# Kernel optimization log

Hardware: AMD Instinct MI355X
Metric: run time of the kernel (lower is better)

The kernel has to match this reference:

```python
import jax, jax.numpy as jnp
import numpy as np

N_NODES = 100000
N_EDGES = 400000
IN_F, HID, OUT_F = 128, 1024, 64


def gcn_conv(x, src, dst, ew, W, b, n):
    # PyG GCNConv: add self-loops (weight 1), symmetric normalization,
    # out[dst] += norm * (x @ W)[src], then bias.
    loop = jnp.arange(n)
    s = jnp.concatenate([src, loop])
    d = jnp.concatenate([dst, loop])
    w = jnp.concatenate([ew, jnp.ones((n,), dtype=ew.dtype)])
    deg = jax.ops.segment_sum(w, d, num_segments=n)
    dinv = jnp.where(deg > 0, jax.lax.rsqrt(deg), 0.0)
    norm = dinv[s] * w * dinv[d]                      # [E+N]
    h = x @ W                                         # [N, out]
    out = jax.ops.segment_sum(h[s] * norm[:, None], d, num_segments=n)
    return out + b


def setup_inputs() -> dict:
    key = jax.random.key(0)
    k = jax.random.split(key, 8)
    x = jax.random.normal(k[0], (N_NODES, IN_F), dtype=jnp.float32)
    edge_index = jax.random.randint(k[1], (2, N_EDGES), 0, N_NODES, dtype=jnp.int64)
    edge_weight = jax.random.uniform(k[2], (N_EDGES,), dtype=jnp.float32)
    # Glorot-ish init for params
    W1 = jax.random.normal(k[3], (IN_F, HID), dtype=jnp.float32) * (1.0 / np.sqrt(IN_F))
    b1 = jnp.zeros((HID,), dtype=jnp.float32)
    W2 = jax.random.normal(k[4], (HID, OUT_F), dtype=jnp.float32) * (1.0 / np.sqrt(HID))
    b2 = jnp.zeros((OUT_F,), dtype=jnp.float32)
    return {"x": x, "edge_index": edge_index, "edge_weight": edge_weight,
            "W1": W1, "b1": b1, "W2": W2, "b2": b2}


def reference(x, edge_index, edge_weight, W1, b1, W2, b2):
    src, dst = edge_index[0], edge_index[1]
    h = gcn_conv(x, src, dst, edge_weight, W1, b1, N_NODES)
    h = jax.nn.relu(h)
    # F.dropout with training=False is identity (eval mode)
    out = gcn_conv(h, src, dst, edge_weight, W2, b2, N_NODES)
    return out
```

## Files before the change

### kernel.cpp

```cpp
#include <hip/hip_runtime.h>
#include <hip/hip_bf16.h>

#define N_NODES 100000
#define N_EDGES 400000
#define IN_F    128
#define HID     1024
#define OUT_F   64
#define BUCKET_CAP 24

typedef __attribute__((ext_vector_type(8))) short short8;
typedef __attribute__((ext_vector_type(4))) float floatx4;

__device__ inline unsigned short f2bf(float f) {
    unsigned int u = __float_as_uint(f);
    unsigned int r = u + 0x7FFF + ((u >> 16) & 1);
    return (unsigned short)(r >> 16);
}

__device__ inline float bf2f(unsigned int lo16) {
    return __uint_as_float(lo16 << 16);
}

__device__ __forceinline__ void gload_lds16(const void* g, void* l) {
    __builtin_amdgcn_global_load_lds(
        (const __attribute__((address_space(1))) void*)g,
        (__attribute__((address_space(3))) void*)l, 16, 0, 0);
}


__global__ void init_kernel(float* __restrict__ deg, int* __restrict__ cnt, int n) {
    int i = blockIdx.x * blockDim.x + threadIdx.x;
    if (i < n) { deg[i] = 1.0f; cnt[i] = 0; }
}

__global__ void deg_accum_kernel(const int* __restrict__ dst, const float* __restrict__ w,
                                 float* __restrict__ deg, int E) {
    int e = blockIdx.x * blockDim.x + threadIdx.x;
    if (e < E) atomicAdd(&deg[dst[e]], w[e]);
}

__global__ void rsqrt_inplace_kernel(float* __restrict__ deg, int n) {
    int i = blockIdx.x * blockDim.x + threadIdx.x;
    if (i < n) deg[i] = rsqrtf(deg[i]);
}

__global__ void fill_pairs_kernel(const int* __restrict__ src, const int* __restrict__ dst,
                                  const float* __restrict__ w, const float* __restrict__ dinv,
                                  int* __restrict__ cnt, int2* __restrict__ pairs, int E) {
    int e = blockIdx.x * blockDim.x + threadIdx.x;
    if (e < E) {
        int s = src[e];
        int d = dst[e];
        float nv = dinv[s] * w[e] * dinv[d];
        int slot = atomicAdd(&cnt[d], 1);
        if (slot < BUCKET_CAP)
            pairs[(long)d * BUCKET_CAP + slot] = make_int2(s, __float_as_int(nv));
    }
}


__global__ __launch_bounds__(256) void gather128_kernel(
    const int2* __restrict__ pairs, const int* __restrict__ cnt,
    const float* __restrict__ dinv, const float* __restrict__ feat,
    unsigned short* __restrict__ xab)
{
    int node = blockIdx.x * 4 + (threadIdx.x >> 6);
    int l = threadIdx.x & 63;
    float di = dinv[node];
    float s = di * di;
    float2 acc = ((const float2*)(feat + (long)node * IN_F))[l];
    acc.x *= s; acc.y *= s;
    int c = cnt[node]; c = c < BUCKET_CAP ? c : BUCKET_CAP;
    const int2* p = pairs + (long)node * BUCKET_CAP;
    int j = 0;
    for (; j + 4 <= c; j += 4) {
        int2 p0 = p[j], p1 = p[j + 1], p2 = p[j + 2], p3 = p[j + 3];
        float2 v0 = ((const float2*)(feat + (long)p0.x * IN_F))[l];
        float2 v1 = ((const float2*)(feat + (long)p1.x * IN_F))[l];
        float2 v2 = ((const float2*)(feat + (long)p2.x * IN_F))[l];
        float2 v3 = ((const float2*)(feat + (long)p3.x * IN_F))[l];
        float n0 = __int_as_float(p0.y), n1 = __int_as_float(p1.y);
        float n2 = __int_as_float(p2.y), n3 = __int_as_float(p3.y);
        acc.x += n0 * v0.x + n1 * v1.x + n2 * v2.x + n3 * v3.x;
        acc.y += n0 * v0.y + n1 * v1.y + n2 * v2.y + n3 * v3.y;
    }
    for (; j < c; j++) {
        int2 pp = p[j];
        float nv = __int_as_float(pp.y);
        float2 v = ((const float2*)(feat + (long)pp.x * IN_F))[l];
        acc.x += nv * v.x; acc.y += nv * v.y;
    }
    unsigned int pk = (unsigned int)f2bf(acc.x) | ((unsigned int)f2bf(acc.y) << 16);
    ((unsigned int*)(xab + (long)node * IN_F))[l] = pk;
}

__global__ __launch_bounds__(256) void gather64_kernel(
    const int2* __restrict__ pairs, const int* __restrict__ cnt,
    const float* __restrict__ dinv, const unsigned short* __restrict__ tb,
    const float* __restrict__ bias, float* __restrict__ out)
{
    int node = blockIdx.x * 8 + (threadIdx.x >> 5);
    int l = threadIdx.x & 31;
    float di = dinv[node];
    float s = di * di;
    unsigned int tv = ((const unsigned int*)(tb + (long)node * OUT_F))[l];
    float2 bb = ((const float2*)bias)[l];
    float2 acc;
    acc.x = bf2f(tv & 0xffffu) * s + bb.x;
    acc.y = bf2f(tv >> 16) * s + bb.y;
    int c = cnt[node]; c = c < BUCKET_CAP ? c : BUCKET_CAP;
    const int2* p = pairs + (long)node * BUCKET_CAP;
    int j = 0;
    for (; j + 4 <= c; j += 4) {
        int2 p0 = p[j], p1 = p[j + 1], p2 = p[j + 2], p3 = p[j + 3];
        unsigned int u0 = ((const unsigned int*)(tb + (long)p0.x * OUT_F))[l];
        unsigned int u1 = ((const unsigned int*)(tb + (long)p1.x * OUT_F))[l];
        unsigned int u2 = ((const unsigned int*)(tb + (long)p2.x * OUT_F))[l];
        unsigned int u3 = ((const unsigned int*)(tb + (long)p3.x * OUT_F))[l];
        float n0 = __int_as_float(p0.y), n1 = __int_as_float(p1.y);
        float n2 = __int_as_float(p2.y), n3 = __int_as_float(p3.y);
        acc.x += n0 * bf2f(u0 & 0xffffu) + n1 * bf2f(u1 & 0xffffu)
               + n2 * bf2f(u2 & 0xffffu) + n3 * bf2f(u3 & 0xffffu);
        acc.y += n0 * bf2f(u0 >> 16) + n1 * bf2f(u1 >> 16)
               + n2 * bf2f(u2 >> 16) + n3 * bf2f(u3 >> 16);
    }
    for (; j < c; j++) {
        int2 pp = p[j];
        float nv = __int_as_float(pp.y);
        unsigned int u = ((const unsigned int*)(tb + (long)pp.x * OUT_F))[l];
        acc.x += nv * bf2f(u & 0xffffu);
        acc.y += nv * bf2f(u >> 16);
    }
    ((float2*)(out + (long)node * OUT_F))[l] = acc;
}


__global__ void convert_wstream_kernel(const float* __restrict__ W1, const float* __restrict__ W2,
                                       unsigned short* __restrict__ S) {
    int r = blockIdx.x * blockDim.x + threadIdx.x;
    int c = blockIdx.y;
    int f = r >> 9;
    int l = (r >> 3) & 63;
    int j = r & 7;
    float v;
    if (f < 16) {
        int nt = f >> 2, kt = f & 3;
        int hid = c * 64 + nt * 16 + (l & 15);
        int k   = kt * 32 + (l >> 4) * 8 + j;
        v = W1[(long)k * HID + hid];
    } else {
        int f2 = f - 16;
        int kb = f2 >> 2, nt = f2 & 3;
        int kh = c * 64 + kb * 32 + (l >> 4) * 8 + j;
        int oc = nt * 16 + (l & 15);
        v = W2[(long)kh * OUT_F + oc];
    }
    S[(long)c * 12288 + r] = f2bf(v);
}


__global__ __launch_bounds__(512, 2) void fused_mlp_mfma_kernel(
    const unsigned short* __restrict__ Xb, const unsigned short* __restrict__ Wstream,
    const float* __restrict__ b1, unsigned short* __restrict__ Tb, int M)
{
    __shared__ unsigned short Wbuf[2][12288];
    __shared__ unsigned short Hs[8][2048];

    const int tid = threadIdx.x;
    const int w   = tid >> 6;
    const int l   = tid & 63;
    const int lr  = l & 15;
    const int lq  = l >> 4;
    const int swz = (lr & 7) << 4;
    const long row0 = (long)blockIdx.x * 256 + w * 32;

    short8 bx[2][4];
    #pragma unroll
    for (int rt = 0; rt < 2; rt++) {
        long row = row0 + rt * 16 + lr;
        if (row < M) {
            const unsigned short* p = Xb + row * IN_F + lq * 8;
            #pragma unroll
            for (int kt = 0; kt < 4; kt++)
                bx[rt][kt] = *(const short8*)(p + kt * 32);
        } else {
            #pragma unroll
            for (int kt = 0; kt < 4; kt++)
                #pragma unroll
                for (int j = 0; j < 8; j++) bx[rt][kt][j] = 0;
        }
    }

    {
        const unsigned short* g = Wstream + (long)(w * 3) * 512 + l * 8;
        unsigned short* d = &Wbuf[0][(w * 3) * 512];
        #pragma unroll
        for (int s = 0; s < 3; s++)
            gload_lds16(g + s * 512, d + s * 512);
    }
    __syncthreads();

    floatx4 tacc[2][4];
    #pragma unroll
    for (int rt = 0; rt < 2; rt++)
        #pragma unroll
        for (int nt = 0; nt < 4; nt++)
            tacc[rt][nt] = (floatx4)0.0f;

    for (int c = 0; c < 16; c++) {
        const int cur = c & 1;

        if (c < 15) {
            const unsigned short* g = Wstream + (long)(c + 1) * 12288 + (long)(w * 3) * 512 + l * 8;
            unsigned short* d = &Wbuf[cur ^ 1][(w * 3) * 512];
            #pragma unroll
            for (int s = 0; s < 3; s++)
                gload_lds16(g + s * 512, d + s * 512);
        }

        const unsigned short* Wb = &Wbuf[cur][0];

        floatx4 hacc[2][4];
        #pragma unroll
        for (int rt = 0; rt < 2; rt++)
            #pragma unroll
            for (int nt = 0; nt < 4; nt++)
                hacc[rt][nt] = (floatx4)0.0f;

        #pragma unroll
        for (int nt = 0; nt < 4; nt++) {
            short8 w1f[4];
            #pragma unroll
            for (int kt = 0; kt < 4; kt++)
                w1f[kt] = *(const short8*)(Wb + (nt * 4 + kt) * 512 + l * 8);
            #pragma unroll
            for (int kt = 0; kt < 4; kt++) {
                hacc[0][nt] = __builtin_amdgcn_mfma_f32_16x16x32_bf16(w1f[kt], bx[0][kt], hacc[0][nt], 0, 0, 0);
                hacc[1][nt] = __builtin_amdgcn_mfma_f32_16x16x32_bf16(w1f[kt], bx[1][kt], hacc[1][nt], 0, 0, 0);
            }
        }

        char* slab = (char*)&Hs[w][0];
        #pragma unroll
        for (int nt = 0; nt < 4; nt++) {
            floatx4 bb = *(const floatx4*)(b1 + c * 64 + nt * 16 + lq * 4);
            #pragma unroll
            for (int rt = 0; rt < 2; rt++) {
                float h0 = fmaxf(hacc[rt][nt][0] + bb[0], 0.0f);
                float h1 = fmaxf(hacc[rt][nt][1] + bb[1], 0.0f);
                float h2 = fmaxf(hacc[rt][nt][2] + bb[2], 0.0f);
                float h3 = fmaxf(hacc[rt][nt][3] + bb[3], 0.0f);
                unsigned int p0 = (unsigned int)f2bf(h0) | ((unsigned int)f2bf(h1) << 16);
                unsigned int p1 = (unsigned int)f2bf(h2) | ((unsigned int)f2bf(h3) << 16);
                int off = (rt * 16 + lr) * 128 + (((nt * 32) + lq * 8) ^ swz);
                *(uint2*)(slab + off) = make_uint2(p0, p1);
            }
        }

        short8 hf[2][2];
        #pragma unroll
        for (int rt = 0; rt < 2; rt++)
            #pragma unroll
            for (int kb = 0; kb < 2; kb++) {
                int off = (rt * 16 + lr) * 128 + ((kb * 64 + lq * 16) ^ swz);
                hf[rt][kb] = *(const short8*)(slab + off);
            }

        #pragma unroll
        for (int kb = 0; kb < 2; kb++) {
            #pragma unroll
            for (int nt = 0; nt < 4; nt++) {
                short8 w2f = *(const short8*)(Wb + (16 + kb * 4 + nt) * 512 + l * 8);
                tacc[0][nt] = __builtin_amdgcn_mfma_f32_16x16x32_bf16(w2f, hf[0][kb], tacc[0][nt], 0, 0, 0);
                tacc[1][nt] = __builtin_amdgcn_mfma_f32_16x16x32_bf16(w2f, hf[1][kb], tacc[1][nt], 0, 0, 0);
            }
        }

        if (c < 15) __syncthreads();
    }

    #pragma unroll
    for (int rt = 0; rt < 2; rt++) {
        long row = row0 + rt * 16 + lr;
        if (row < M) {
            #pragma unroll
            for (int nt = 0; nt < 4; nt++) {
                unsigned int q0 = (unsigned int)f2bf(tacc[rt][nt][0]) | ((unsigned int)f2bf(tacc[rt][nt][1]) << 16);
                unsigned int q1 = (unsigned int)f2bf(tacc[rt][nt][2]) | ((unsigned int)f2bf(tacc[rt][nt][3]) << 16);
                *(uint2*)(Tb + row * OUT_F + nt * 16 + lq * 4) = make_uint2(q0, q1);
            }
        }
    }
}


extern "C" void kernel_launch(void* const* d_in, const int* in_sizes, int n_in,
                              void* d_out, int out_size, void* d_ws, size_t ws_size,
                              hipStream_t stream) {
    const float* x   = (const float*)d_in[0];
    const int*   src = (const int*)d_in[1];
    const int*   dst = ((const int*)d_in[1]) + N_EDGES;
    const float* ew  = (const float*)d_in[2];
    const float* W1  = (const float*)d_in[3];
    const float* b1  = (const float*)d_in[4];
    const float* W2  = (const float*)d_in[5];
    const float* b2  = (const float*)d_in[6];
    float* out = (float*)d_out;

    float* ws     = (float*)d_ws;
    float* dinv   = ws;
    int*   cnt    = (int*)(ws + 100096);
    int2*  pairs  = (int2*)(ws + 200192);
    unsigned short* xab = (unsigned short*)(ws + 5000192);
    unsigned short* tb  = (unsigned short*)(ws + 11400192);
    unsigned short* wstream = (unsigned short*)(ws + 14600192);

    const int B = 256;

    init_kernel<<<(N_NODES + B - 1) / B, B, 0, stream>>>(dinv, cnt, N_NODES);
    deg_accum_kernel<<<(N_EDGES + B - 1) / B, B, 0, stream>>>(dst, ew, dinv, N_EDGES);
    convert_wstream_kernel<<<dim3(48, 16), B, 0, stream>>>(W1, W2, wstream);
    rsqrt_inplace_kernel<<<(N_NODES + B - 1) / B, B, 0, stream>>>(dinv, N_NODES);
    fill_pairs_kernel<<<(N_EDGES + B - 1) / B, B, 0, stream>>>(src, dst, ew, dinv, cnt, pairs, N_EDGES);

    gather128_kernel<<<N_NODES / 4, 256, 0, stream>>>(pairs, cnt, dinv, x, xab);

    fused_mlp_mfma_kernel<<<(N_NODES + 255) / 256, 512, 0, stream>>>(
        xab, wstream, b1, tb, N_NODES);

    gather64_kernel<<<N_NODES / 8, 256, 0, stream>>>(pairs, cnt, dinv, tb, b2, out);
}
```

Baseline: 182.0 us.

## Pre-convert x to bf16 for gather and double rows per wave in fused MLP

Adds a kernel that converts the input features to bf16 once, so the first-layer neighbour gather reads half as many bytes per edge. The fused MLP kernel now processes 64 rows per wave (512 per block) instead of 32. Each W1/W2 fragment loaded from LDS is reused across four row tiles, and the hidden accumulator is restructured per output-column tile to keep register use bounded. The cost is an extra conversion pass over x and more LDS and register pressure, which may lower occupancy. Grid size halves, to about 196 blocks for 100k nodes.

```diff
diff --git a/kernel.cpp b/kernel.cpp
--- a/kernel.cpp
+++ b/kernel.cpp
@@ -59,36 +59,55 @@
 }
 
 
+__global__ void convert_xb_kernel(const float* __restrict__ in, unsigned short* __restrict__ out, long n8) {
+    long i = (long)blockIdx.x * blockDim.x + threadIdx.x;
+    if (i < n8) {
+        float4 a = ((const float4*)in)[i * 2];
+        float4 b = ((const float4*)in)[i * 2 + 1];
+        unsigned int q0 = (unsigned int)f2bf(a.x) | ((unsigned int)f2bf(a.y) << 16);
+        unsigned int q1 = (unsigned int)f2bf(a.z) | ((unsigned int)f2bf(a.w) << 16);
+        unsigned int q2 = (unsigned int)f2bf(b.x) | ((unsigned int)f2bf(b.y) << 16);
+        unsigned int q3 = (unsigned int)f2bf(b.z) | ((unsigned int)f2bf(b.w) << 16);
+        ((uint4*)out)[i] = make_uint4(q0, q1, q2, q3);
+    }
+}
+
+
 __global__ __launch_bounds__(256) void gather128_kernel(
     const int2* __restrict__ pairs, const int* __restrict__ cnt,
-    const float* __restrict__ dinv, const float* __restrict__ feat,
+    const float* __restrict__ dinv, const unsigned short* __restrict__ xb,
     unsigned short* __restrict__ xab)
 {
     int node = blockIdx.x * 4 + (threadIdx.x >> 6);
     int l = threadIdx.x & 63;
     float di = dinv[node];
     float s = di * di;
-    float2 acc = ((const float2*)(feat + (long)node * IN_F))[l];
-    acc.x *= s; acc.y *= s;
+    unsigned int uv = ((const unsigned int*)(xb + (long)node * IN_F))[l];
+    float2 acc;
+    acc.x = bf2f(uv & 0xffffu) * s;
+    acc.y = bf2f(uv >> 16) * s;
     int c = cnt[node]; c = c < BUCKET_CAP ? c : BUCKET_CAP;
     const int2* p = pairs + (long)node * BUCKET_CAP;
     int j = 0;
     for (; j + 4 <= c; j += 4) {
         int2 p0 = p[j], p1 = p[j + 1], p2 = p[j + 2], p3 = p[j + 3];
-        float2 v0 = ((const float2*)(feat + (long)p0.x * IN_F))[l];
-        float2 v1 = ((const float2*)(feat + (long)p1.x * IN_F))[l];
-        float2 v2 = ((const float2*)(feat + (long)p2.x * IN_F))[l];
-        float2 v3 = ((const float2*)(feat + (long)p3.x * IN_F))[l];
+        unsigned int u0 = ((const unsigned int*)(xb + (long)p0.x * IN_F))[l];
+        unsigned int u1 = ((const unsigned int*)(xb + (long)p1.x * IN_F))[l];
+        unsigned int u2 = ((const unsigned int*)(xb + (long)p2.x * IN_F))[l];
+        unsigned int u3 = ((const unsigned int*)(xb + (long)p3.x * IN_F))[l];
         float n0 = __int_as_float(p0.y), n1 = __int_as_float(p1.y);
         float n2 = __int_as_float(p2.y), n3 = __int_as_float(p3.y);
-        acc.x += n0 * v0.x + n1 * v1.x + n2 * v2.x + n3 * v3.x;
-        acc.y += n0 * v0.y + n1 * v1.y + n2 * v2.y + n3 * v3.y;
+        acc.x += n0 * bf2f(u0 & 0xffffu) + n1 * bf2f(u1 & 0xffffu)
+               + n2 * bf2f(u2 & 0xffffu) + n3 * bf2f(u3 & 0xffffu);
+        acc.y += n0 * bf2f(u0 >> 16) + n1 * bf2f(u1 >> 16)
+               + n2 * bf2f(u2 >> 16) + n3 * bf2f(u3 >> 16);
     }
     for (; j < c; j++) {
         int2 pp = p[j];
         float nv = __int_as_float(pp.y);
-        float2 v = ((const float2*)(feat + (long)pp.x * IN_F))[l];
-        acc.x += nv * v.x; acc.y += nv * v.y;
+        unsigned int u = ((const unsigned int*)(xb + (long)pp.x * IN_F))[l];
+        acc.x += nv * bf2f(u & 0xffffu);
+        acc.y += nv * bf2f(u >> 16);
     }
     unsigned int pk = (unsigned int)f2bf(acc.x) | ((unsigned int)f2bf(acc.y) << 16);
     ((unsigned int*)(xab + (long)node * IN_F))[l] = pk;
@@ -164,7 +183,7 @@
     const float* __restrict__ b1, unsigned short* __restrict__ Tb, int M)
 {
     __shared__ unsigned short Wbuf[2][12288];
-    __shared__ unsigned short Hs[8][2048];
+    __shared__ unsigned short Hs[8][4096];
 
     const int tid = threadIdx.x;
     const int w   = tid >> 6;
@@ -172,11 +191,11 @@
     const int lr  = l & 15;
     const int lq  = l >> 4;
     const int swz = (lr & 7) << 4;
-    const long row0 = (long)blockIdx.x * 256 + w * 32;
-
-    short8 bx[2][4];
+    const long row0 = (long)blockIdx.x * 512 + w * 64;
+
+    short8 bx[4][4];
     #pragma unroll
-    for (int rt = 0; rt < 2; rt++) {
+    for (int rt = 0; rt < 4; rt++) {
         long row = row0 + rt * 16 + lr;
         if (row < M) {
             const unsigned short* p = Xb + row * IN_F + lq * 8;
@@ -200,9 +219,9 @@
     }
     __syncthreads();
 
-    floatx4 tacc[2][4];
+    floatx4 tacc[4][4];
     #pragma unroll
-    for (int rt = 0; rt < 2; rt++)
+    for (int rt = 0; rt < 4; rt++)
         #pragma unroll
         for (int nt = 0; nt < 4; nt++)
             tacc[rt][nt] = (floatx4)0.0f;
@@ -219,13 +238,7 @@
         }
 
         const unsigned short* Wb = &Wbuf[cur][0];
-
-        floatx4 hacc[2][4];
-        #pragma unroll
-        for (int rt = 0; rt < 2; rt++)
-            #pragma unroll
-            for (int nt = 0; nt < 4; nt++)
-                hacc[rt][nt] = (floatx4)0.0f;
+        char* slab = (char*)&Hs[w][0];
 
         #pragma unroll
         for (int nt = 0; nt < 4; nt++) {
@@ -233,23 +246,24 @@
             #pragma unroll
             for (int kt = 0; kt < 4; kt++)
                 w1f[kt] = *(const short8*)(Wb + (nt * 4 + kt) * 512 + l * 8);
-            #pragma unroll
-            for (int kt = 0; kt < 4; kt++) {
-                hacc[0][nt] = __builtin_amdgcn_mfma_f32_16x16x32_bf16(w1f[kt], bx[0][kt], hacc[0][nt], 0, 0, 0);
-                hacc[1][nt] = __builtin_amdgcn_mfma_f32_16x16x32_bf16(w1f[kt], bx[1][kt], hacc[1][nt], 0, 0, 0);
-            }
-        }
-
-        char* slab = (char*)&Hs[w][0];
-        #pragma unroll
-        for (int nt = 0; nt < 4; nt++) {
+
+            floatx4 hacc[4];
+            #pragma unroll
+            for (int rt = 0; rt < 4; rt++) hacc[rt] = (floatx4)0.0f;
+
+            #pragma unroll
+            for (int kt = 0; kt < 4; kt++)
+                #pragma unroll
+                for (int rt = 0; rt < 4; rt++)
+                    hacc[rt] = __builtin_amdgcn_mfma_f32_16x16x32_bf16(w1f[kt], bx[rt][kt], hacc[rt], 0, 0, 0);
+
             floatx4 bb = *(const floatx4*)(b1 + c * 64 + nt * 16 + lq * 4);
             #pragma unroll
-            for (int rt = 0; rt < 2; rt++) {
-                float h0 = fmaxf(hacc[rt][nt][0] + bb[0], 0.0f);
-                float h1 = fmaxf(hacc[rt][nt][1] + bb[1], 0.0f);
-                float h2 = fmaxf(hacc[rt][nt][2] + bb[2], 0.0f);
-                float h3 = fmaxf(hacc[rt][nt][3] + bb[3], 0.0f);
+            for (int rt = 0; rt < 4; rt++) {
+                float h0 = fmaxf(hacc[rt][0] + bb[0], 0.0f);
+                float h1 = fmaxf(hacc[rt][1] + bb[1], 0.0f);
+                float h2 = fmaxf(hacc[rt][2] + bb[2], 0.0f);
+                float h3 = fmaxf(hacc[rt][3] + bb[3], 0.0f);
                 unsigned int p0 = (unsigned int)f2bf(h0) | ((unsigned int)f2bf(h1) << 16);
                 unsigned int p1 = (unsigned int)f2bf(h2) | ((unsigned int)f2bf(h3) << 16);
                 int off = (rt * 16 + lr) * 128 + (((nt * 32) + lq * 8) ^ swz);
@@ -257,9 +271,9 @@
             }
         }
 
-        short8 hf[2][2];
-        #pragma unroll
-        for (int rt = 0; rt < 2; rt++)
+        short8 hf[4][2];
+        #pragma unroll
+        for (int rt = 0; rt < 4; rt++)
             #pragma unroll
             for (int kb = 0; kb < 2; kb++) {
                 int off = (rt * 16 + lr) * 128 + ((kb * 64 + lq * 16) ^ swz);
@@ -271,8 +285,9 @@
             #pragma unroll
             for (int nt = 0; nt < 4; nt++) {
                 short8 w2f = *(const short8*)(Wb + (16 + kb * 4 + nt) * 512 + l * 8);
-                tacc[0][nt] = __builtin_amdgcn_mfma_f32_16x16x32_bf16(w2f, hf[0][kb], tacc[0][nt], 0, 0, 0);
-                tacc[1][nt] = __builtin_amdgcn_mfma_f32_16x16x32_bf16(w2f, hf[1][kb], tacc[1][nt], 0, 0, 0);
+                #pragma unroll
+                for (int rt = 0; rt < 4; rt++)
+                    tacc[rt][nt] = __builtin_amdgcn_mfma_f32_16x16x32_bf16(w2f, hf[rt][kb], tacc[rt][nt], 0, 0, 0);
             }
         }
 
@@ -280,7 +295,7 @@
     }
 
     #pragma unroll
-    for (int rt = 0; rt < 2; rt++) {
+    for (int rt = 0; rt < 4; rt++) {
         long row = row0 + rt * 16 + lr;
         if (row < M) {
             #pragma unroll
@@ -311,21 +326,24 @@
     float* dinv   = ws;
     int*   cnt    = (int*)(ws + 100096);
     int2*  pairs  = (int2*)(ws + 200192);
-    unsigned short* xab = (unsigned short*)(ws + 5000192);
-    unsigned short* tb  = (unsigned short*)(ws + 11400192);
-    unsigned short* wstream = (unsigned short*)(ws + 14600192);
+    unsigned short* xb  = (unsigned short*)(ws + 5000192);
+    unsigned short* xab = (unsigned short*)(ws + 11400192);
+    unsigned short* tb  = (unsigned short*)(ws + 17800192);
+    unsigned short* wstream = (unsigned short*)(ws + 21000192);
 
     const int B = 256;
 
     init_kernel<<<(N_NODES + B - 1) / B, B, 0, stream>>>(dinv, cnt, N_NODES);
     deg_accum_kernel<<<(N_EDGES + B - 1) / B, B, 0, stream>>>(dst, ew, dinv, N_EDGES);
+    convert_xb_kernel<<<(int)(((long)N_NODES * IN_F / 8 + B - 1) / B), B, 0, stream>>>(
+        x, xb, (long)N_NODES * IN_F / 8);
     convert_wstream_kernel<<<dim3(48, 16), B, 0, stream>>>(W1, W2, wstream);
     rsqrt_inplace_kernel<<<(N_NODES + B - 1) / B, B, 0, stream>>>(dinv, N_NODES);
     fill_pairs_kernel<<<(N_EDGES + B - 1) / B, B, 0, stream>>>(src, dst, ew, dinv, cnt, pairs, N_EDGES);
 
-    gather128_kernel<<<N_NODES / 4, 256, 0, stream>>>(pairs, cnt, dinv, x, xab);
-
-    fused_mlp_mfma_kernel<<<(N_NODES + 255) / 256, 512, 0, stream>>>(
+    gather128_kernel<<<N_NODES / 4, 256, 0, stream>>>(pairs, cnt, dinv, xb, xab);
+
+    fused_mlp_mfma_kernel<<<(N_NODES + 511) / 512, 512, 0, stream>>>(
         xab, wstream, b1, tb, N_NODES);
 
     gather64_kernel<<<N_NODES / 8, 256, 0, stream>>>(pairs, cnt, dinv, tb, b2, out);
```

After: 188.7 us. 3.7% more time.
